# Kernel tuning notes

Measured on AMD Instinct MI355X. Metric: run time of the kernel, lower is better.

Reference implementation:

```python
import jax, jax.numpy as jnp
import numpy as np
import math

ACCBLOCK = 32
SPLITS = 2


def _mam(x, w, accblock):
    """MAM fully-connected: block-accumulate products along K, then max+min over blocks.
    x: [M, K], w: [K, N]  ->  [M, N] = max_blk(partial) + min_blk(partial)
    Implemented as a scan over blocks with running max/min to avoid a [M, nblk, N] tensor.
    """
    M, K = x.shape
    N = w.shape[1]
    nblk = K // accblock
    assert nblk * accblock == K
    xb = x.reshape(M, nblk, accblock).transpose(1, 0, 2)  # [nblk, M, B]
    wb = w.reshape(nblk, accblock, N)                      # [nblk, B, N]
    big = jnp.asarray(jnp.finfo(x.dtype).max, x.dtype)

    def step(carry, blk):
        mx, mn = carry
        xi, wi = blk                      # [M, B], [B, N]
        s = xi @ wi                       # block partial sum [M, N]
        return (jnp.maximum(mx, s), jnp.minimum(mn, s)), None

    init = (jnp.full((M, N), -big, x.dtype), jnp.full((M, N), big, x.dtype))
    (mx, mn), _ = jax.lax.scan(step, init, (xb, wb))
    return mx + mn


def reference(x, weight, bias):
    # eval mode, vcon_steps=0 -> alpha=1, beta=0; no weight dropout, no output dropout
    in_features = weight.shape[1]
    w = weight.T  # [K, N]
    sub = math.ceil(in_features / SPLITS)
    last = in_features - sub * (SPLITS - 1)
    out = _mam(x[:, :sub], w[:sub], ACCBLOCK)
    for i in range(1, SPLITS - 1):
        out = out + _mam(x[:, i * sub:(i + 1) * sub], w[i * sub:(i + 1) * sub], ACCBLOCK)
    out = out + _mam(x[:, in_features - last:], w[in_features - last:], ACCBLOCK)
    return out + bias[None, :]


def setup_inputs() -> dict:
    key = jax.random.key(0)
    k1, k2, k3 = jax.random.split(key, 3)
    M, K, N = 2048, 4096, 4096
    x = jax.random.normal(k1, (M, K), dtype=jnp.float32)
    weight = jax.random.normal(k2, (N, K), dtype=jnp.float32) * (1.0 / math.sqrt(K))
    bias = jax.random.normal(k3, (N,), dtype=jnp.float32) * (1.0 / math.sqrt(K))
    return {"x": x, "weight": weight, "bias": bias}
```

## Files before the change

### kernel.cpp

```cpp
#include <hip/hip_runtime.h>
#include <cstdint>
#include <cstddef>

typedef __bf16 bf16;
typedef __bf16 bf16x4 __attribute__((ext_vector_type(4)));
typedef __bf16 bf16x8 __attribute__((ext_vector_type(8)));
typedef float  f32x4  __attribute__((ext_vector_type(4)));

#define MDIM 2048
#define NDIM 4096
#define KDIM 4096
#define FLOATMAX 3.402823466e38f

__global__ void cvt_f32_to_bf16(const float* __restrict__ src,
                                bf16* __restrict__ dst, int n4) {
    int i = blockIdx.x * blockDim.x + threadIdx.x;
    const int stride = gridDim.x * blockDim.x;
    for (; i < n4; i += stride) {
        f32x4 v = reinterpret_cast<const f32x4*>(src)[i];
        reinterpret_cast<bf16x4*>(dst)[i] = __builtin_convertvector(v, bf16x4);
    }
}

__device__ __forceinline__ void g2lds16(const bf16* g, bf16* l) {
    __builtin_amdgcn_global_load_lds(
        (const __attribute__((address_space(1))) uint32_t*)g,
        (__attribute__((address_space(3))) uint32_t*)l, 16, 0, 0);
}

__global__ __launch_bounds__(512, 2) void mam_kernel(
    const bf16* __restrict__ A,
    const bf16* __restrict__ B,
    const float* __restrict__ bias,
    float* __restrict__ out)
{
    __shared__ __align__(16) bf16 sA0[128 * 32];
    __shared__ __align__(16) bf16 sA1[128 * 32];
    __shared__ __align__(16) bf16 sB0[128 * 32];
    __shared__ __align__(16) bf16 sB1[128 * 32];

    const int t    = threadIdx.x;
    const int lane = t & 63;
    const int w    = t >> 6;
    const int wm   = (w >> 2) * 64;
    const int wn   = (w & 3) * 32;

    const int m0 = blockIdx.y * 128;
    const int n0 = blockIdx.x * 128;

    const int srow  = t >> 2;
    const int skoff = (t & 3) * 8;
    const bf16* gA = A + (size_t)(m0 + srow) * KDIM + skoff;
    const bf16* gB = B + (size_t)(n0 + srow) * KDIM + skoff;
    bf16* lA0 = &sA0[t * 8];
    bf16* lA1 = &sA1[t * 8];
    bf16* lB0 = &sB0[t * 8];
    bf16* lB1 = &sB1[t * 8];

    const int frow = lane & 15;
    const int fk   = (lane >> 4) * 8;

    const f32x4 kZero = {0.f, 0.f, 0.f, 0.f};

    f32x4 acc[4][2];
#pragma unroll
    for (int i = 0; i < 4; ++i)
#pragma unroll
        for (int j = 0; j < 2; ++j) acc[i][j] = kZero;

#pragma unroll 1
    for (int split = 0; split < 2; ++split) {
        f32x4 mx[4][2], mn[4][2];
#pragma unroll
        for (int i = 0; i < 4; ++i)
#pragma unroll
            for (int j = 0; j < 2; ++j) {
                mx[i][j] = (f32x4)(-FLOATMAX);
                mn[i][j] = (f32x4)(FLOATMAX);
            }

        const bf16* gAs = gA + (size_t)split * 2048;
        const bf16* gBs = gB + (size_t)split * 2048;

#pragma unroll 1
        for (int bb = 0; bb < 32; ++bb) {
            __syncthreads();
            const bf16* ga = gAs + (size_t)bb * 64;
            const bf16* gb = gBs + (size_t)bb * 64;
            g2lds16(ga,      lA0);
            g2lds16(ga + 32, lA1);
            g2lds16(gb,      lB0);
            g2lds16(gb + 32, lB1);
            __syncthreads();

            bf16x8 aF0[4], aF1[4], bF0[2], bF1[2];
#pragma unroll
            for (int i = 0; i < 4; ++i) {
                const int off = (wm + i * 16 + frow) * 32 + fk;
                aF0[i] = *(const bf16x8*)&sA0[off];
                aF1[i] = *(const bf16x8*)&sA1[off];
            }
#pragma unroll
            for (int j = 0; j < 2; ++j) {
                const int off = (wn + j * 16 + frow) * 32 + fk;
                bF0[j] = *(const bf16x8*)&sB0[off];
                bF1[j] = *(const bf16x8*)&sB1[off];
            }

#pragma unroll
            for (int i = 0; i < 4; ++i) {
#pragma unroll
                for (int j = 0; j < 2; ++j) {
                    f32x4 s0 = __builtin_amdgcn_mfma_f32_16x16x32_bf16(
                        aF0[i], bF0[j], kZero, 0, 0, 0);
                    f32x4 s1 = __builtin_amdgcn_mfma_f32_16x16x32_bf16(
                        aF1[i], bF1[j], kZero, 0, 0, 0);
#pragma unroll
                    for (int r = 0; r < 4; ++r) {
                        mx[i][j][r] = fmaxf(fmaxf(mx[i][j][r], s0[r]), s1[r]);
                        mn[i][j][r] = fminf(fminf(mn[i][j][r], s0[r]), s1[r]);
                    }
                }
            }
        }

#pragma unroll
        for (int i = 0; i < 4; ++i)
#pragma unroll
            for (int j = 0; j < 2; ++j)
                acc[i][j] += mx[i][j] + mn[i][j];
    }

    const int orow = (lane >> 4) * 4;
    const int ocol = lane & 15;
#pragma unroll
    for (int j = 0; j < 2; ++j) {
        const int col = n0 + wn + j * 16 + ocol;
        const float bv = bias[col];
#pragma unroll
        for (int i = 0; i < 4; ++i) {
            const int row = m0 + wm + i * 16 + orow;
#pragma unroll
            for (int r = 0; r < 4; ++r) {
                out[(size_t)(row + r) * NDIM + col] = acc[i][j][r] + bv;
            }
        }
    }
}

extern "C" void kernel_launch(void* const* d_in, const int* in_sizes, int n_in,
                              void* d_out, int out_size, void* d_ws, size_t ws_size,
                              hipStream_t stream) {
    const float* x    = (const float*)d_in[0];
    const float* wgt  = (const float*)d_in[1];
    const float* bias = (const float*)d_in[2];
    float* out = (float*)d_out;

    bf16* xbf = (bf16*)d_ws;
    bf16* wbf = xbf + (size_t)MDIM * KDIM;

    const int xn4 = (MDIM * KDIM) / 4;
    const int wn4 = (NDIM * KDIM) / 4;
    cvt_f32_to_bf16<<<dim3(2048), dim3(256), 0, stream>>>(x, xbf, xn4);
    cvt_f32_to_bf16<<<dim3(2048), dim3(256), 0, stream>>>(wgt, wbf, wn4);

    dim3 grid(NDIM / 128, MDIM / 128);
    mam_kernel<<<grid, dim3(512), 0, stream>>>(xbf, wbf, bias, out);
}
```

Measured before the change: 294.0 us.

## Double-buffer LDS tiles, XOR-swizzle LDS layout, and fuse the bf16 conversion kernels

Result: faster. 253.9 us (-13.6%).

```diff
diff --git a/kernel.cpp b/kernel.cpp
--- a/kernel.cpp
+++ b/kernel.cpp
@@ -12,13 +12,18 @@
 #define KDIM 4096
 #define FLOATMAX 3.402823466e38f
 
-__global__ void cvt_f32_to_bf16(const float* __restrict__ src,
-                                bf16* __restrict__ dst, int n4) {
+__global__ void cvt2_f32_to_bf16(const float* __restrict__ x, const float* __restrict__ w,
+                                 bf16* __restrict__ xb, bf16* __restrict__ wb,
+                                 int xn4, int wn4) {
+    const int stride = gridDim.x * blockDim.x;
     int i = blockIdx.x * blockDim.x + threadIdx.x;
-    const int stride = gridDim.x * blockDim.x;
-    for (; i < n4; i += stride) {
-        f32x4 v = reinterpret_cast<const f32x4*>(src)[i];
-        reinterpret_cast<bf16x4*>(dst)[i] = __builtin_convertvector(v, bf16x4);
+    for (int k = i; k < xn4; k += stride) {
+        f32x4 v = reinterpret_cast<const f32x4*>(x)[k];
+        reinterpret_cast<bf16x4*>(xb)[k] = __builtin_convertvector(v, bf16x4);
+    }
+    for (int k = i; k < wn4; k += stride) {
+        f32x4 v = reinterpret_cast<const f32x4*>(w)[k];
+        reinterpret_cast<bf16x4*>(wb)[k] = __builtin_convertvector(v, bf16x4);
     }
 }
 
@@ -34,10 +39,8 @@
     const float* __restrict__ bias,
     float* __restrict__ out)
 {
-    __shared__ __align__(16) bf16 sA0[128 * 32];
-    __shared__ __align__(16) bf16 sA1[128 * 32];
-    __shared__ __align__(16) bf16 sB0[128 * 32];
-    __shared__ __align__(16) bf16 sB1[128 * 32];
+    __shared__ __align__(16) bf16 sA[2][2][128 * 32];
+    __shared__ __align__(16) bf16 sB[2][2][128 * 32];
 
     const int t    = threadIdx.x;
     const int lane = t & 63;
@@ -48,87 +51,102 @@
     const int m0 = blockIdx.y * 128;
     const int n0 = blockIdx.x * 128;
 
-    const int srow  = t >> 2;
-    const int skoff = (t & 3) * 8;
-    const bf16* gA = A + (size_t)(m0 + srow) * KDIM + skoff;
-    const bf16* gB = B + (size_t)(n0 + srow) * KDIM + skoff;
-    bf16* lA0 = &sA0[t * 8];
-    bf16* lA1 = &sA1[t * 8];
-    bf16* lB0 = &sB0[t * 8];
-    bf16* lB1 = &sB1[t * 8];
+    const int srow   = t >> 2;
+    const int spos   = t & 3;
+    const int schunk = spos ^ ((srow >> 1) & 3);
+    const bf16* gA = A + (size_t)(m0 + srow) * KDIM + schunk * 8;
+    const bf16* gB = B + (size_t)(n0 + srow) * KDIM + schunk * 8;
+    const int ldst = t * 8;
 
     const int frow = lane & 15;
-    const int fk   = (lane >> 4) * 8;
+    const int q    = lane >> 4;
+    int offA[4], offB[2];
+#pragma unroll
+    for (int i = 0; i < 4; ++i) {
+        const int R = wm + i * 16 + frow;
+        offA[i] = R * 32 + (q ^ ((R >> 1) & 3)) * 8;
+    }
+#pragma unroll
+    for (int j = 0; j < 2; ++j) {
+        const int R = wn + j * 16 + frow;
+        offB[j] = R * 32 + (q ^ ((R >> 1) & 3)) * 8;
+    }
 
     const f32x4 kZero = {0.f, 0.f, 0.f, 0.f};
 
-    f32x4 acc[4][2];
+    f32x4 acc[4][2], mx[4][2], mn[4][2];
 #pragma unroll
     for (int i = 0; i < 4; ++i)
 #pragma unroll
-        for (int j = 0; j < 2; ++j) acc[i][j] = kZero;
+        for (int j = 0; j < 2; ++j) {
+            acc[i][j] = kZero;
+            mx[i][j] = (f32x4)(-FLOATMAX);
+            mn[i][j] = (f32x4)(FLOATMAX);
+        }
 
-#pragma unroll 1
-    for (int split = 0; split < 2; ++split) {
-        f32x4 mx[4][2], mn[4][2];
+    auto prefetch = [&](int s, int pb) {
+        const bf16* ga = gA + (size_t)s * 64;
+        const bf16* gb = gB + (size_t)s * 64;
+        g2lds16(ga,      &sA[pb][0][ldst]);
+        g2lds16(ga + 32, &sA[pb][1][ldst]);
+        g2lds16(gb,      &sB[pb][0][ldst]);
+        g2lds16(gb + 32, &sB[pb][1][ldst]);
+    };
+
+    auto compute = [&](int pb) {
+        bf16x8 aF0[4], aF1[4], bF0[2], bF1[2];
+#pragma unroll
+        for (int i = 0; i < 4; ++i) {
+            aF0[i] = *(const bf16x8*)&sA[pb][0][offA[i]];
+            aF1[i] = *(const bf16x8*)&sA[pb][1][offA[i]];
+        }
+#pragma unroll
+        for (int j = 0; j < 2; ++j) {
+            bF0[j] = *(const bf16x8*)&sB[pb][0][offB[j]];
+            bF1[j] = *(const bf16x8*)&sB[pb][1][offB[j]];
+        }
+#pragma unroll
+        for (int i = 0; i < 4; ++i) {
+#pragma unroll
+            for (int j = 0; j < 2; ++j) {
+                f32x4 s0 = __builtin_amdgcn_mfma_f32_16x16x32_bf16(
+                    aF0[i], bF0[j], kZero, 0, 0, 0);
+                f32x4 s1 = __builtin_amdgcn_mfma_f32_16x16x32_bf16(
+                    aF1[i], bF1[j], kZero, 0, 0, 0);
+#pragma unroll
+                for (int r = 0; r < 4; ++r) {
+                    mx[i][j][r] = fmaxf(fmaxf(mx[i][j][r], s0[r]), s1[r]);
+                    mn[i][j][r] = fminf(fminf(mn[i][j][r], s0[r]), s1[r]);
+                }
+            }
+        }
+    };
+
+    auto split_reset = [&]() {
 #pragma unroll
         for (int i = 0; i < 4; ++i)
 #pragma unroll
             for (int j = 0; j < 2; ++j) {
+                acc[i][j] += mx[i][j] + mn[i][j];
                 mx[i][j] = (f32x4)(-FLOATMAX);
                 mn[i][j] = (f32x4)(FLOATMAX);
             }
+    };
 
-        const bf16* gAs = gA + (size_t)split * 2048;
-        const bf16* gBs = gB + (size_t)split * 2048;
+    prefetch(0, 0);
 
+    int bb = 0;
 #pragma unroll 1
-        for (int bb = 0; bb < 32; ++bb) {
-            __syncthreads();
-            const bf16* ga = gAs + (size_t)bb * 64;
-            const bf16* gb = gBs + (size_t)bb * 64;
-            g2lds16(ga,      lA0);
-            g2lds16(ga + 32, lA1);
-            g2lds16(gb,      lB0);
-            g2lds16(gb + 32, lB1);
-            __syncthreads();
-
-            bf16x8 aF0[4], aF1[4], bF0[2], bF1[2];
-#pragma unroll
-            for (int i = 0; i < 4; ++i) {
-                const int off = (wm + i * 16 + frow) * 32 + fk;
-                aF0[i] = *(const bf16x8*)&sA0[off];
-                aF1[i] = *(const bf16x8*)&sA1[off];
-            }
-#pragma unroll
-            for (int j = 0; j < 2; ++j) {
-                const int off = (wn + j * 16 + frow) * 32 + fk;
-                bF0[j] = *(const bf16x8*)&sB0[off];
-                bF1[j] = *(const bf16x8*)&sB1[off];
-            }
-
-#pragma unroll
-            for (int i = 0; i < 4; ++i) {
-#pragma unroll
-                for (int j = 0; j < 2; ++j) {
-                    f32x4 s0 = __builtin_amdgcn_mfma_f32_16x16x32_bf16(
-                        aF0[i], bF0[j], kZero, 0, 0, 0);
-                    f32x4 s1 = __builtin_amdgcn_mfma_f32_16x16x32_bf16(
-                        aF1[i], bF1[j], kZero, 0, 0, 0);
-#pragma unroll
-                    for (int r = 0; r < 4; ++r) {
-                        mx[i][j][r] = fmaxf(fmaxf(mx[i][j][r], s0[r]), s1[r]);
-                        mn[i][j][r] = fminf(fminf(mn[i][j][r], s0[r]), s1[r]);
-                    }
-                }
-            }
-        }
-
-#pragma unroll
-        for (int i = 0; i < 4; ++i)
-#pragma unroll
-            for (int j = 0; j < 2; ++j)
-                acc[i][j] += mx[i][j] + mn[i][j];
+    for (int it = 0; it < 32; ++it) {
+        __syncthreads();
+        prefetch(bb + 1, 1);
+        compute(0);
+        ++bb;
+        __syncthreads();
+        if (bb < 63) prefetch(bb + 1, 0);
+        compute(1);
+        if (bb == 31 || bb == 63) split_reset();
+        ++bb;
     }
 
     const int orow = (lane >> 4) * 4;
@@ -161,8 +179,7 @@
 
     const int xn4 = (MDIM * KDIM) / 4;
     const int wn4 = (NDIM * KDIM) / 4;
-    cvt_f32_to_bf16<<<dim3(2048), dim3(256), 0, stream>>>(x, xbf, xn4);
-    cvt_f32_to_bf16<<<dim3(2048), dim3(256), 0, stream>>>(wgt, wbf, wn4);
+    cvt2_f32_to_bf16<<<dim3(4096), dim3(256), 0, stream>>>(x, wgt, xbf, wbf, xn4, wn4);
 
     dim3 grid(NDIM / 128, MDIM / 128);
     mam_kernel<<<grid, dim3(512), 0, stream>>>(xbf, wbf, bias, out);
```
